# Performance work log

Measured on AMD Instinct MI355X. Metric: run time of the kernel, lower is better.

The kernel has to match this reference:

```python
import jax, jax.numpy as jnp
import numpy as np

O, NI, F, D, NN, M = 2048, 16, 4, 128, 8, 8  # outfits, item slots, factors, dim, neighbors, valid slots
D2 = D // 2

def lrelu(x):
    return jax.nn.leaky_relu(x, 0.01)

def mlp2(x, W1, b1, W2, b2):
    # Linear -> LeakyReLU -> Linear -> LeakyReLU (Dropout is identity at inference)
    return lrelu(lrelu(x @ W1 + b1) @ W2 + b2)

def setup_inputs():
    ks = jax.random.split(jax.random.key(0), 16)
    s = 0.05
    pos = jnp.arange(NI)[None, :]
    outfit_items = jnp.where(pos < M, jax.random.randint(ks[0], (O, NI), 0, NI), -1)
    items_neighbor = jax.random.randint(ks[1], (O, NI, NN), -1, NI)
    items_feature = jax.random.normal(ks[2], (O, NI, D), dtype=jnp.float32)
    items_factors = jnp.zeros((O, NI, F, D), dtype=jnp.float32)
    p = {
        'cf_W1': jax.random.normal(ks[3], (F, D, D2)) * s,
        'cf_b1': jnp.zeros((F, D2)),
        'cf_W2': jax.random.normal(ks[4], (F, D2, D)) * s,
        'cf_b2': jnp.zeros((F, D)),
        'f2f_W1': jax.random.normal(ks[5], (D, D)) * s, 'f2f_b1': jnp.zeros((D,)),
        'f2f_W2': jax.random.normal(ks[6], (D, D)) * s, 'f2f_b2': jnp.zeros((D,)),
        'f2i_W1': jax.random.normal(ks[7], (D, D)) * s, 'f2i_b1': jnp.zeros((D,)),
        'f2i_W2': jax.random.normal(ks[8], (D, D)) * s, 'f2i_b2': jnp.zeros((D,)),
        'i2i_W1': jax.random.normal(ks[9], (D, D)) * s, 'i2i_b1': jnp.zeros((D,)),
        'i2i_W2': jax.random.normal(ks[10], (D, D)) * s, 'i2i_b2': jnp.zeros((D,)),
        'o2s_W': jax.random.normal(ks[11], (D, 1)) * s, 'o2s_b': jnp.zeros((1,)),
    }
    return dict(outfit_items=outfit_items, items_feature=items_feature,
                items_neighbor=items_neighbor, items_factors=items_factors, **p)

def _forward(outfit_items, items_feature, items_neighbor, items_factors,
             cf_W1, cf_b1, cf_W2, cf_b2, f2f_W1, f2f_b1, f2f_W2, f2f_b2,
             f2i_W1, f2i_b1, f2i_W2, f2i_b2, i2i_W1, i2i_b1, i2i_W2, i2i_b2,
             o2s_W, o2s_b):
    del items_factors  # creat_factors overwrites every entry in the original
    # --- creat_factors: per-factor 2-layer MLP on every item feature -> [O,NI,F,D]
    h = lrelu(jnp.einsum('oid,fde->oife', items_feature, cf_W1) + cf_b1)
    fac = lrelu(jnp.einsum('oife,fed->oifd', h, cf_W2) + cf_b2)

    # --- inter_factors: sequential over outfit slots; later slots read updated factors
    def outfit_fac(fac_o, oi_o, nbr_o):
        def step(f, i):
            valid = i != -1
            ic = jnp.maximum(i, 0)
            cand = jnp.concatenate([oi_o, nbr_o[ic]])                # [NI+NN]
            cm = (cand != -1) & (cand != i) & valid
            t = f[ic]                                                # [F,D] snapshot
            msg = mlp2(t[None] * f[jnp.maximum(cand, 0)],
                       f2f_W1, f2f_b1, f2f_W2, f2f_b2)               # [NI+NN,F,D]
            add = jnp.sum(jnp.where(cm[:, None, None], msg, 0.0), axis=0)
            return f.at[ic].add(jnp.where(valid, add, 0.0)), None
        f, _ = jax.lax.scan(step, fac_o, oi_o)
        return f
    fac = jax.vmap(outfit_fac)(fac, outfit_items, items_neighbor)

    # --- infer_items: feature[i] += sum_j f2i(fac[i,j]) for outfit members
    g = mlp2(fac, f2i_W1, f2i_b1, f2i_W2, f2i_b2).sum(axis=2)        # [O,NI,D]
    ic = jnp.maximum(outfit_items, 0)
    w = (outfit_items != -1).astype(g.dtype)                          # [O,NI]
    gsel = jnp.take_along_axis(g, ic[..., None], axis=1)
    scat = jax.vmap(lambda gs, idx, ww: jnp.zeros((NI, D), gs.dtype).at[idx].add(ww[:, None] * gs))
    feat = items_feature + scat(gsel, ic, w)

    # --- inter_items: sequential; current value detached (.data in original)
    def outfit_feat(fo_init, oi_o):
        jc = jnp.maximum(oi_o, 0)
        def step(fo, i):
            valid = i != -1
            ic_ = jnp.maximum(i, 0)
            t = jax.lax.stop_gradient(fo[ic_])
            msgs = mlp2(fo[jc], i2i_W1, i2i_b1, i2i_W2, i2i_b2)      # [NI,D]
            m = ((oi_o != -1) & (oi_o != i)).astype(fo.dtype)
            new = t + jnp.sum(m[:, None] * msgs, axis=0)
            return jnp.where(valid, fo.at[ic_].set(new), fo), None
        fo, _ = jax.lax.scan(step, fo_init, oi_o)
        return fo
    feat = jax.vmap(outfit_feat)(feat, outfit_items)

    # --- infer_outfit + score
    fsel = jnp.take_along_axis(feat, ic[..., None], axis=1)
    outfits = jnp.sum(w[..., None] * fsel, axis=1)                    # [O,D]
    scores = jax.nn.sigmoid(outfits @ o2s_W + o2s_b)[:, 0]            # [O]

    # --- com_loss: ||F F^T - I||_F^2 over valid slots (positional mask), / n_outfits
    G = jnp.einsum('oifd,oigd->oifg', fac, fac) - jnp.eye(F, dtype=fac.dtype)
    com = jnp.sum(w * jnp.sum(G * G, axis=(-1, -2))) / O
    return scores, jnp.reshape(com, (1,))

def reference(outfit_items, items_feature, items_neighbor, items_factors,
              cf_W1, cf_b1, cf_W2, cf_b2, f2f_W1, f2f_b1, f2f_W2, f2f_b2,
              f2i_W1, f2i_b1, f2i_W2, f2i_b2, i2i_W1, i2i_b1, i2i_W2, i2i_b2,
              o2s_W, o2s_b):
    return _forward(outfit_items, items_feature, items_neighbor, items_factors,
                    cf_W1, cf_b1, cf_W2, cf_b2, f2f_W1, f2f_b1, f2f_W2, f2f_b2,
                    f2i_W1, f2i_b1, f2i_W2, f2i_b2, i2i_W1, i2i_b1, i2i_W2, i2i_b2,
                    o2s_W, o2s_b)
```

## Files before the change

### kernel.cpp

```cpp
#include <hip/hip_runtime.h>
#include <hip/hip_bf16.h>
#include <math.h>


typedef __attribute__((ext_vector_type(8))) short short8;
typedef __attribute__((ext_vector_type(4))) float f32x4;

#define MFMA16(a, b, c) __builtin_amdgcn_mfma_f32_16x16x32_bf16(a, b, c, 0, 0, 0)

__device__ __forceinline__ float lrelu(float x) { return x > 0.0f ? x : 0.01f * x; }

__device__ __forceinline__ ushort f2bf(float f) {
  unsigned u = __builtin_bit_cast(unsigned, f);
  u += 0x7fffu + ((u >> 16) & 1u);
  return (ushort)(u >> 16);
}
__device__ __forceinline__ float bflo(unsigned u) {
  return __builtin_bit_cast(float, u << 16);
}
__device__ __forceinline__ unsigned pk2(float a, float b) {
  float2 t; t.x = a; t.y = b;
  __hip_bfloat162 h = __float22bfloat162_rn(t);
  unsigned u;
  __builtin_memcpy(&u, &h, 4);
  return u;
}
__device__ __forceinline__ short8 load_bfrag(const float* __restrict__ W, int ldn,
                                             int kbase, int col) {
  short8 r;
#pragma unroll
  for (int j = 0; j < 8; ++j) r[j] = (short)f2bf(W[(kbase + j) * ldn + col]);
  return r;
}

__global__ void zero_com(float* out) { if (threadIdx.x == 0) out[2048] = 0.0f; }

__global__ __launch_bounds__(512, 4) void mfgn_kernel(
    const int* __restrict__ outfit_items,
    const float* __restrict__ items_feature,
    const int* __restrict__ items_neighbor,
    const float* __restrict__ cfW1, const float* __restrict__ cfb1,
    const float* __restrict__ cfW2, const float* __restrict__ cfb2,
    const float* __restrict__ f2fW1, const float* __restrict__ f2fb1,
    const float* __restrict__ f2fW2, const float* __restrict__ f2fb2,
    const float* __restrict__ f2iW1, const float* __restrict__ f2ib1,
    const float* __restrict__ f2iW2, const float* __restrict__ f2ib2,
    const float* __restrict__ i2iW1, const float* __restrict__ i2ib1,
    const float* __restrict__ i2iW2, const float* __restrict__ i2ib2,
    const float* __restrict__ o2sW, const float* __restrict__ o2sb,
    float* __restrict__ out)
{
  __shared__ float facL[16 * 528];
  __shared__ ushort prodS[64 * 136] __attribute__((aligned(16)));
  __shared__ ushort hidS[64 * 136] __attribute__((aligned(16)));
  __shared__ ushort featB[16 * 136] __attribute__((aligned(16)));
  __shared__ float redE[8];
  __shared__ int oiL[16];
  __shared__ int clAll[256];
  __shared__ int ncAll[16];
  __shared__ int vslL[16];
  __shared__ int refcntL[16];
  __shared__ int nvsL;

  const int o = blockIdx.x;
  const int tid = (int)threadIdx.x;
  const int lane = tid & 63;
  const int wid = tid >> 6;
  const int n16 = lane & 15;
  const int q = lane >> 4;
  const int kb = q * 8;
  const int col = wid * 16 + n16;

  if (tid < 16) oiL[tid] = outfit_items[o * 16 + tid];
  {
    const int n = tid >> 5, d0 = (tid & 31) * 4;
    float4 v = *(const float4*)(items_feature + o * 2048 + tid * 4);
    uint2 pk; pk.x = pk2(v.x, v.y); pk.y = pk2(v.z, v.w);
    *(uint2*)(featB + n * 136 + d0) = pk;
  }
  if (tid == 0) {
    int cnt = 0;
    for (int s = 0; s < 16; ++s) refcntL[s] = 0;
    for (int s = 0; s < 16; ++s) {
      int v = oiL[s];
      if (v != -1) { vslL[cnt++] = s; refcntL[v]++; }
    }
    nvsL = cnt;
  }
  for (int s = wid; s < 16; s += 8) {
    const int iv = outfit_items[o * 16 + s];
    if (iv == -1) { if (lane == 0) ncAll[s] = 0; continue; }
    int cand = -1;
    if (lane < 24) cand = (lane < 16) ? outfit_items[o * 16 + lane]
                                      : items_neighbor[o * 128 + iv * 8 + (lane - 16)];
    bool ok = (lane < 24) && (cand != -1) && (cand != iv);
    unsigned long long bm = __ballot(ok);
    if (ok) clAll[s * 16 + __popcll(bm & ((1ull << lane) - 1ull))] = cand;
    if (lane == 0) ncAll[s] = (int)__popcll(bm);
  }
  __syncthreads();
  const int nvs = nvsL;

  {
    const int f = wid & 3, half = wid >> 2;
    short8 wA[2][4];
#pragma unroll
    for (int etl = 0; etl < 2; ++etl)
#pragma unroll
      for (int kt = 0; kt < 4; ++kt)
        wA[etl][kt] = load_bfrag(cfW1 + f * 8192, 64, kt * 32 + kb, (half * 2 + etl) * 16 + n16);
    f32x4 acc[2];
    acc[0] = (f32x4){0.f,0.f,0.f,0.f}; acc[1] = (f32x4){0.f,0.f,0.f,0.f};
    for (int kt = 0; kt < 4; ++kt) {
      short8 x = *(const short8*)(featB + n16 * 136 + kt * 32 + kb);
      acc[0] = MFMA16(wA[0][kt], x, acc[0]);
      acc[1] = MFMA16(wA[1][kt], x, acc[1]);
    }
#pragma unroll
    for (int etl = 0; etl < 2; ++etl) {
      f32x4 b1q = *(const f32x4*)(cfb1 + f * 64 + (half * 2 + etl) * 16 + q * 4);
      float h0 = lrelu(acc[etl][0] + b1q[0]), h1 = lrelu(acc[etl][1] + b1q[1]);
      float h2 = lrelu(acc[etl][2] + b1q[2]), h3 = lrelu(acc[etl][3] + b1q[3]);
      uint2 pk; pk.x = pk2(h0, h1); pk.y = pk2(h2, h3);
      *(uint2*)(hidS + (f * 16 + n16) * 136 + (half * 2 + etl) * 16 + q * 4) = pk;
    }
    __syncthreads();
    short8 wB[4][2];
#pragma unroll
    for (int ctl = 0; ctl < 4; ++ctl)
#pragma unroll
      for (int kt = 0; kt < 2; ++kt)
        wB[ctl][kt] = load_bfrag(cfW2 + f * 8192, 128, kt * 32 + kb, half * 64 + ctl * 16 + n16);
    f32x4 acc2[4];
#pragma unroll
    for (int ctl = 0; ctl < 4; ++ctl) acc2[ctl] = (f32x4){0.f,0.f,0.f,0.f};
    for (int kt = 0; kt < 2; ++kt) {
      short8 h = *(const short8*)(hidS + (f * 16 + n16) * 136 + kt * 32 + kb);
#pragma unroll
      for (int ctl = 0; ctl < 4; ++ctl) acc2[ctl] = MFMA16(h, wB[ctl][kt], acc2[ctl]);
    }
#pragma unroll
    for (int ctl = 0; ctl < 4; ++ctl) {
      int c = half * 64 + ctl * 16 + n16;
      float b2 = cfb2[f * 128 + c];
#pragma unroll
      for (int r = 0; r < 4; ++r)
        facL[(q * 4 + r) * 528 + f * 132 + c] = lrelu(acc2[ctl][r] + b2);
    }
    __syncthreads();
  }

  {
    short8 w1f[4], w2f[4];
#pragma unroll
    for (int kt = 0; kt < 4; ++kt) {
      w1f[kt] = load_bfrag(f2fW1, 128, kt * 32 + kb, col);
      w2f[kt] = load_bfrag(f2fW2, 128, kt * 32 + kb, col);
    }
    const f32x4 b1q = *(const f32x4*)(f2fb1 + wid * 16 + q * 4);
    const float b2v = f2fb2[col];
    const int rS = tid >> 3, kcS = tid & 7;
    const int fS = rS & 3, ciS = rS >> 2;
    const int k0 = kcS * 16;

    for (int s = 0; s < 16; ++s) {
      const int iv = oiL[s];
      if (iv == -1) continue;
      const int nc = ncAll[s];
      const int mtn = (nc + 3) >> 2;
      if (ciS < nc) {
        const int cit = clAll[s * 16 + ciS];
        const float* tp = facL + iv * 528 + fS * 132;
        const float* cp = facL + cit * 528 + fS * 132;
#pragma unroll
        for (int i2 = 0; i2 < 2; ++i2) {
          const int k = k0 + i2 * 8;
          float4 a0 = *(const float4*)(tp + k), a1 = *(const float4*)(tp + k + 4);
          float4 c0 = *(const float4*)(cp + k), c1 = *(const float4*)(cp + k + 4);
          uint4 u;
          u.x = pk2(a0.x * c0.x, a0.y * c0.y); u.y = pk2(a0.z * c0.z, a0.w * c0.w);
          u.z = pk2(a1.x * c1.x, a1.y * c1.y); u.w = pk2(a1.z * c1.z, a1.w * c1.w);
          *(uint4*)(prodS + rS * 136 + k) = u;
        }
      } else if (ciS < mtn * 4) {
        uint4 z; z.x = z.y = z.z = z.w = 0;
        *(uint4*)(prodS + rS * 136 + k0) = z;
        *(uint4*)(prodS + rS * 136 + k0 + 8) = z;
      }
      __syncthreads();
      for (int mt = 0; mt < mtn; ++mt) {
        f32x4 acc = (f32x4){0.f,0.f,0.f,0.f};
#pragma unroll
        for (int kt = 0; kt < 4; ++kt) {
          short8 x = *(const short8*)(prodS + (mt * 16 + n16) * 136 + kt * 32 + kb);
          acc = MFMA16(w1f[kt], x, acc);
        }
        float h0 = lrelu(acc[0] + b1q[0]), h1 = lrelu(acc[1] + b1q[1]);
        float h2 = lrelu(acc[2] + b1q[2]), h3 = lrelu(acc[3] + b1q[3]);
        uint2 pk; pk.x = pk2(h0, h1); pk.y = pk2(h2, h3);
        *(uint2*)(hidS + (mt * 16 + n16) * 136 + wid * 16 + q * 4) = pk;
      }
      __syncthreads();
      float part[4] = {0.f, 0.f, 0.f, 0.f};
      for (int mt = 0; mt < mtn; ++mt) {
        f32x4 acc2 = (f32x4){0.f,0.f,0.f,0.f};
#pragma unroll
        for (int kt = 0; kt < 4; ++kt) {
          short8 h = *(const short8*)(hidS + (mt * 16 + n16) * 136 + kt * 32 + kb);
          acc2 = MFMA16(h, w2f[kt], acc2);
        }
        bool act = (mt * 4 + q) < nc;
        if (act) {
#pragma unroll
          for (int r = 0; r < 4; ++r) part[r] += lrelu(acc2[r] + b2v);
        }
      }
#pragma unroll
      for (int r = 0; r < 4; ++r) {
        float v = part[r];
        v += __shfl_xor(v, 16);
        v += __shfl_xor(v, 32);
        part[r] = v;
      }
      if (q == 0) {
#pragma unroll
        for (int r = 0; r < 4; ++r)
          facL[iv * 528 + r * 132 + col] += part[r];
      }
      __syncthreads();
    }
  }

  {
    short8 w1f[4], w2f[4];
#pragma unroll
    for (int kt = 0; kt < 4; ++kt) {
      w1f[kt] = load_bfrag(f2iW1, 128, kt * 32 + kb, col);
      w2f[kt] = load_bfrag(f2iW2, 128, kt * 32 + kb, col);
    }
    const f32x4 b1q = *(const f32x4*)(f2ib1 + wid * 16 + q * 4);
    const float b2v = f2ib2[col];
    {
      const int r = tid >> 3, kc = tid & 7, k0 = kc * 16;
      const int f = r & 3, item = r >> 2;
      const float* sp = facL + item * 528 + f * 132;
#pragma unroll
      for (int i2 = 0; i2 < 2; ++i2) {
        const int k = k0 + i2 * 8;
        float4 a0 = *(const float4*)(sp + k), a1 = *(const float4*)(sp + k + 4);
        uint4 u;
        u.x = pk2(a0.x, a0.y); u.y = pk2(a0.z, a0.w);
        u.z = pk2(a1.x, a1.y); u.w = pk2(a1.z, a1.w);
        *(uint4*)(prodS + r * 136 + k) = u;
      }
    }
    __syncthreads();
    f32x4 acc[4];
#pragma unroll
    for (int mt = 0; mt < 4; ++mt) acc[mt] = (f32x4){0.f,0.f,0.f,0.f};
    for (int kt = 0; kt < 4; ++kt)
#pragma unroll
      for (int mt = 0; mt < 4; ++mt) {
        short8 x = *(const short8*)(prodS + (mt * 16 + n16) * 136 + kt * 32 + kb);
        acc[mt] = MFMA16(w1f[kt], x, acc[mt]);
      }
#pragma unroll
    for (int mt = 0; mt < 4; ++mt) {
      float h0 = lrelu(acc[mt][0] + b1q[0]), h1 = lrelu(acc[mt][1] + b1q[1]);
      float h2 = lrelu(acc[mt][2] + b1q[2]), h3 = lrelu(acc[mt][3] + b1q[3]);
      uint2 pk; pk.x = pk2(h0, h1); pk.y = pk2(h2, h3);
      *(uint2*)(hidS + (mt * 16 + n16) * 136 + wid * 16 + q * 4) = pk;
    }
    __syncthreads();
    f32x4 acc2[4];
#pragma unroll
    for (int mt = 0; mt < 4; ++mt) acc2[mt] = (f32x4){0.f,0.f,0.f,0.f};
    for (int kt = 0; kt < 4; ++kt)
#pragma unroll
      for (int mt = 0; mt < 4; ++mt) {
        short8 h = *(const short8*)(hidS + (mt * 16 + n16) * 136 + kt * 32 + kb);
        acc2[mt] = MFMA16(h, w2f[kt], acc2[mt]);
      }
#pragma unroll
    for (int mt = 0; mt < 4; ++mt) {
      int item = mt * 4 + q;
      float g = 0.f;
#pragma unroll
      for (int r = 0; r < 4; ++r) g += lrelu(acc2[mt][r] + b2v);
      int a = item * 136 + col;
      featB[a] = f2bf(bflo((unsigned)featB[a]) + (float)refcntL[item] * g);
    }
    __syncthreads();
  }

  {
    short8 w1f[4], w2f[4];
#pragma unroll
    for (int kt = 0; kt < 4; ++kt) {
      w1f[kt] = load_bfrag(i2iW1, 128, kt * 32 + kb, col);
      w2f[kt] = load_bfrag(i2iW2, 128, kt * 32 + kb, col);
    }
    const f32x4 b1q = *(const f32x4*)(i2ib1 + wid * 16 + q * 4);
    const float b2v = i2ib2[col];

    for (int u = 0; u < nvs; ++u) {
      const int iv = oiL[vslL[u]];
      f32x4 acc = (f32x4){0.f,0.f,0.f,0.f};
      for (int kt = 0; kt < 4; ++kt) {
        short8 x = *(const short8*)(featB + n16 * 136 + kt * 32 + kb);
        acc = MFMA16(w1f[kt], x, acc);
      }
      {
        float h0 = lrelu(acc[0] + b1q[0]), h1 = lrelu(acc[1] + b1q[1]);
        float h2 = lrelu(acc[2] + b1q[2]), h3 = lrelu(acc[3] + b1q[3]);
        uint2 pk; pk.x = pk2(h0, h1); pk.y = pk2(h2, h3);
        *(uint2*)(hidS + n16 * 136 + wid * 16 + q * 4) = pk;
      }
      __syncthreads();
      f32x4 acc2 = (f32x4){0.f,0.f,0.f,0.f};
      for (int kt = 0; kt < 4; ++kt) {
        short8 h = *(const short8*)(hidS + n16 * 136 + kt * 32 + kb);
        acc2 = MFMA16(h, w2f[kt], acc2);
      }
      float part = 0.f;
#pragma unroll
      for (int r = 0; r < 4; ++r) {
        int item = q * 4 + r;
        float w = (item == iv) ? 0.0f : (float)refcntL[item];
        part += w * lrelu(acc2[r] + b2v);
      }
      part += __shfl_xor(part, 16);
      part += __shfl_xor(part, 32);
      if (q == 0) {
        int a = iv * 136 + col;
        featB[a] = f2bf(bflo((unsigned)featB[a]) + part);
      }
      __syncthreads();
    }
  }

  if (tid < 128) {
    float sum = 0.0f;
    for (int u = 0; u < nvs; ++u)
      sum += bflo((unsigned)featB[oiL[vslL[u]] * 136 + tid]);
    float v = sum * o2sW[tid];
#pragma unroll
    for (int off = 1; off < 64; off <<= 1) v += __shfl_xor(v, off);
    if (lane == 0) redE[wid] = v;
  }
  __syncthreads();
  if (tid == 0) {
    float t = redE[0] + redE[1] + o2sb[0];
    out[o] = 1.0f / (1.0f + expf(-t));
  }

  {
    const int n = tid >> 5, f = (tid >> 3) & 3, g = (tid >> 1) & 3, h = tid & 1;
    const float* pa = facL + n * 528 + f * 132 + h * 64;
    const float* pb = facL + n * 528 + g * 132 + h * 64;
    float dot = 0.0f;
    for (int i = 0; i < 16; ++i) {
      float4 a = *(const float4*)(pa + i * 4);
      float4 b = *(const float4*)(pb + i * 4);
      dot += a.x * b.x + a.y * b.y + a.z * b.z + a.w * b.w;
    }
    dot += __shfl_xor(dot, 1);
    float v = dot - ((f == g) ? 1.0f : 0.0f);
    float sq = (h == 0 && oiL[n] != -1) ? v * v : 0.0f;
#pragma unroll
    for (int off = 1; off < 64; off <<= 1) sq += __shfl_xor(sq, off);
    __syncthreads();
    if (lane == 0) redE[wid] = sq;
    __syncthreads();
    if (tid == 0) {
      float tot = 0.f;
#pragma unroll
      for (int w = 0; w < 8; ++w) tot += redE[w];
      atomicAdd(out + 2048, tot * (1.0f / 2048.0f));
    }
  }
}

extern "C" void kernel_launch(void* const* d_in, const int* in_sizes, int n_in,
                              void* d_out, int out_size, void* d_ws, size_t ws_size,
                              hipStream_t stream) {
  float* out = (float*)d_out;
  hipLaunchKernelGGL(zero_com, dim3(1), dim3(64), 0, stream, out);
  hipLaunchKernelGGL(mfgn_kernel, dim3(2048), dim3(512), 0, stream,
                     (const int*)d_in[0],
                     (const float*)d_in[1],
                     (const int*)d_in[2],
                     (const float*)d_in[4], (const float*)d_in[5],
                     (const float*)d_in[6], (const float*)d_in[7],
                     (const float*)d_in[8], (const float*)d_in[9],
                     (const float*)d_in[10], (const float*)d_in[11],
                     (const float*)d_in[12], (const float*)d_in[13],
                     (const float*)d_in[14], (const float*)d_in[15],
                     (const float*)d_in[16], (const float*)d_in[17],
                     (const float*)d_in[18], (const float*)d_in[19],
                     (const float*)d_in[20], (const float*)d_in[21],
                     out);
}
```

Before: 346.7 us.

## Pre-convert weights to transposed bf16 in workspace via a prep kernel

Adds a prep kernel that converts every MLP weight matrix to bf16 once per call, stored transposed in the workspace so each MFMA B/A fragment becomes one contiguous 16-byte load. Before this, each block did 8 strided scalar fp32 loads plus a conversion per fragment, across all 2048 blocks. The prep kernel also takes over zeroing the com output. The f2f loop now walks only the valid slots list instead of skipping -1 slots. The cost is one extra small kernel and a workspace dependency.

```diff
diff --git a/kernel.cpp b/kernel.cpp
--- a/kernel.cpp
+++ b/kernel.cpp
@@ -25,29 +25,45 @@
   __builtin_memcpy(&u, &h, 4);
   return u;
 }
-__device__ __forceinline__ short8 load_bfrag(const float* __restrict__ W, int ldn,
-                                             int kbase, int col) {
-  short8 r;
-#pragma unroll
-  for (int j = 0; j < 8; ++j) r[j] = (short)f2bf(W[(kbase + j) * ldn + col]);
-  return r;
-}
-
-__global__ void zero_com(float* out) { if (threadIdx.x == 0) out[2048] = 0.0f; }
+
+
+__global__ __launch_bounds__(256) void prep_weights(
+    const float* __restrict__ cfW1, const float* __restrict__ cfW2,
+    const float* __restrict__ f2fW1, const float* __restrict__ f2fW2,
+    const float* __restrict__ f2iW1, const float* __restrict__ f2iW2,
+    const float* __restrict__ i2iW1, const float* __restrict__ i2iW2,
+    ushort* __restrict__ ws, float* __restrict__ out) {
+  const int idx = (int)(blockIdx.x * 256 + threadIdx.x);
+  if (idx == 0) out[2048] = 0.0f;
+  float v;
+  if (idx < 32768) {
+    int f = idx >> 13, r = idx & 8191, n = r >> 7, k = r & 127;
+    v = cfW1[f * 8192 + k * 64 + n];
+  } else if (idx < 65536) {
+    int t = idx - 32768;
+    int f = t >> 13, r = t & 8191, n = r >> 6, k = r & 63;
+    v = cfW2[f * 8192 + k * 128 + n];
+  } else {
+    int t = idx - 65536;
+    int seg = t >> 14, r = t & 16383, n = r >> 7, k = r & 127;
+    const float* W = (seg == 0) ? f2fW1 : (seg == 1) ? f2fW2 :
+                     (seg == 2) ? f2iW1 : (seg == 3) ? f2iW2 :
+                     (seg == 4) ? i2iW1 : i2iW2;
+    v = W[k * 128 + n];
+  }
+  ws[idx] = f2bf(v);
+}
 
 __global__ __launch_bounds__(512, 4) void mfgn_kernel(
     const int* __restrict__ outfit_items,
     const float* __restrict__ items_feature,
     const int* __restrict__ items_neighbor,
-    const float* __restrict__ cfW1, const float* __restrict__ cfb1,
-    const float* __restrict__ cfW2, const float* __restrict__ cfb2,
-    const float* __restrict__ f2fW1, const float* __restrict__ f2fb1,
-    const float* __restrict__ f2fW2, const float* __restrict__ f2fb2,
-    const float* __restrict__ f2iW1, const float* __restrict__ f2ib1,
-    const float* __restrict__ f2iW2, const float* __restrict__ f2ib2,
-    const float* __restrict__ i2iW1, const float* __restrict__ i2ib1,
-    const float* __restrict__ i2iW2, const float* __restrict__ i2ib2,
+    const float* __restrict__ cfb1, const float* __restrict__ cfb2,
+    const float* __restrict__ f2fb1, const float* __restrict__ f2fb2,
+    const float* __restrict__ f2ib1, const float* __restrict__ f2ib2,
+    const float* __restrict__ i2ib1, const float* __restrict__ i2ib2,
     const float* __restrict__ o2sW, const float* __restrict__ o2sb,
+    const ushort* __restrict__ wsW,
     float* __restrict__ out)
 {
   __shared__ float facL[16 * 528];
@@ -108,7 +124,8 @@
     for (int etl = 0; etl < 2; ++etl)
 #pragma unroll
       for (int kt = 0; kt < 4; ++kt)
-        wA[etl][kt] = load_bfrag(cfW1 + f * 8192, 64, kt * 32 + kb, (half * 2 + etl) * 16 + n16);
+        wA[etl][kt] = *(const short8*)(wsW + (f * 64 + (half * 2 + etl) * 16 + n16) * 128
+                                       + kt * 32 + kb);
     f32x4 acc[2];
     acc[0] = (f32x4){0.f,0.f,0.f,0.f}; acc[1] = (f32x4){0.f,0.f,0.f,0.f};
     for (int kt = 0; kt < 4; ++kt) {
@@ -130,7 +147,8 @@
     for (int ctl = 0; ctl < 4; ++ctl)
 #pragma unroll
       for (int kt = 0; kt < 2; ++kt)
-        wB[ctl][kt] = load_bfrag(cfW2 + f * 8192, 128, kt * 32 + kb, half * 64 + ctl * 16 + n16);
+        wB[ctl][kt] = *(const short8*)(wsW + 32768 + (f * 128 + half * 64 + ctl * 16 + n16) * 64
+                                       + kt * 32 + kb);
     f32x4 acc2[4];
 #pragma unroll
     for (int ctl = 0; ctl < 4; ++ctl) acc2[ctl] = (f32x4){0.f,0.f,0.f,0.f};
@@ -154,8 +172,8 @@
     short8 w1f[4], w2f[4];
 #pragma unroll
     for (int kt = 0; kt < 4; ++kt) {
-      w1f[kt] = load_bfrag(f2fW1, 128, kt * 32 + kb, col);
-      w2f[kt] = load_bfrag(f2fW2, 128, kt * 32 + kb, col);
+      w1f[kt] = *(const short8*)(wsW + 65536 + col * 128 + kt * 32 + kb);
+      w2f[kt] = *(const short8*)(wsW + 81920 + col * 128 + kt * 32 + kb);
     }
     const f32x4 b1q = *(const f32x4*)(f2fb1 + wid * 16 + q * 4);
     const float b2v = f2fb2[col];
@@ -163,9 +181,9 @@
     const int fS = rS & 3, ciS = rS >> 2;
     const int k0 = kcS * 16;
 
-    for (int s = 0; s < 16; ++s) {
+    for (int u = 0; u < nvs; ++u) {
+      const int s = vslL[u];
       const int iv = oiL[s];
-      if (iv == -1) continue;
       const int nc = ncAll[s];
       const int mtn = (nc + 3) >> 2;
       if (ciS < nc) {
@@ -177,10 +195,10 @@
           const int k = k0 + i2 * 8;
           float4 a0 = *(const float4*)(tp + k), a1 = *(const float4*)(tp + k + 4);
           float4 c0 = *(const float4*)(cp + k), c1 = *(const float4*)(cp + k + 4);
-          uint4 u;
-          u.x = pk2(a0.x * c0.x, a0.y * c0.y); u.y = pk2(a0.z * c0.z, a0.w * c0.w);
-          u.z = pk2(a1.x * c1.x, a1.y * c1.y); u.w = pk2(a1.z * c1.z, a1.w * c1.w);
-          *(uint4*)(prodS + rS * 136 + k) = u;
+          uint4 u4;
+          u4.x = pk2(a0.x * c0.x, a0.y * c0.y); u4.y = pk2(a0.z * c0.z, a0.w * c0.w);
+          u4.z = pk2(a1.x * c1.x, a1.y * c1.y); u4.w = pk2(a1.z * c1.z, a1.w * c1.w);
+          *(uint4*)(prodS + rS * 136 + k) = u4;
         }
       } else if (ciS < mtn * 4) {
         uint4 z; z.x = z.y = z.z = z.w = 0;
@@ -235,8 +253,8 @@
     short8 w1f[4], w2f[4];
 #pragma unroll
     for (int kt = 0; kt < 4; ++kt) {
-      w1f[kt] = load_bfrag(f2iW1, 128, kt * 32 + kb, col);
-      w2f[kt] = load_bfrag(f2iW2, 128, kt * 32 + kb, col);
+      w1f[kt] = *(const short8*)(wsW + 98304 + col * 128 + kt * 32 + kb);
+      w2f[kt] = *(const short8*)(wsW + 114688 + col * 128 + kt * 32 + kb);
     }
     const f32x4 b1q = *(const f32x4*)(f2ib1 + wid * 16 + q * 4);
     const float b2v = f2ib2[col];
@@ -297,8 +315,8 @@
     short8 w1f[4], w2f[4];
 #pragma unroll
     for (int kt = 0; kt < 4; ++kt) {
-      w1f[kt] = load_bfrag(i2iW1, 128, kt * 32 + kb, col);
-      w2f[kt] = load_bfrag(i2iW2, 128, kt * 32 + kb, col);
+      w1f[kt] = *(const short8*)(wsW + 131072 + col * 128 + kt * 32 + kb);
+      w2f[kt] = *(const short8*)(wsW + 147456 + col * 128 + kt * 32 + kb);
     }
     const f32x4 b1q = *(const f32x4*)(i2ib1 + wid * 16 + q * 4);
     const float b2v = i2ib2[col];
@@ -385,19 +403,22 @@
                               void* d_out, int out_size, void* d_ws, size_t ws_size,
                               hipStream_t stream) {
   float* out = (float*)d_out;
-  hipLaunchKernelGGL(zero_com, dim3(1), dim3(64), 0, stream, out);
+  ushort* ws = (ushort*)d_ws;
+  hipLaunchKernelGGL(prep_weights, dim3(640), dim3(256), 0, stream,
+                     (const float*)d_in[4], (const float*)d_in[6],
+                     (const float*)d_in[8], (const float*)d_in[10],
+                     (const float*)d_in[12], (const float*)d_in[14],
+                     (const float*)d_in[16], (const float*)d_in[18],
+                     ws, out);
   hipLaunchKernelGGL(mfgn_kernel, dim3(2048), dim3(512), 0, stream,
                      (const int*)d_in[0],
                      (const float*)d_in[1],
                      (const int*)d_in[2],
-                     (const float*)d_in[4], (const float*)d_in[5],
-                     (const float*)d_in[6], (const float*)d_in[7],
-                     (const float*)d_in[8], (const float*)d_in[9],
-                     (const float*)d_in[10], (const float*)d_in[11],
-                     (const float*)d_in[12], (const float*)d_in[13],
-                     (const float*)d_in[14], (const float*)d_in[15],
-                     (const float*)d_in[16], (const float*)d_in[17],
-                     (const float*)d_in[18], (const float*)d_in[19],
+                     (const float*)d_in[5], (const float*)d_in[7],
+                     (const float*)d_in[9], (const float*)d_in[11],
+                     (const float*)d_in[13], (const float*)d_in[15],
+                     (const float*)d_in[17], (const float*)d_in[19],
                      (const float*)d_in[20], (const float*)d_in[21],
+                     (const ushort*)ws,
                      out);
 }
```

Result: no change. 340.4 us (-1.8%).
